# Performance work log

Hardware: AMD Instinct MI355X
Metric: run time of the kernel (lower is better)

The kernel has to match this reference:

```python
import jax, jax.numpy as jnp
import numpy as np

C = 64
CQ = C // 8
B, D, H, W = 4, 16, 16, 16


def setup_inputs() -> dict:
    key = jax.random.key(0)
    ks = jax.random.split(key, 8)
    s = 1.0 / np.sqrt(C)
    return {
        "x": jax.random.normal(ks[0], (B, C, D, H, W), jnp.float32),
        "Wq": jax.random.normal(ks[1], (CQ, C), jnp.float32) * s,
        "bq": jax.random.normal(ks[2], (CQ,), jnp.float32) * 0.01,
        "Wk": jax.random.normal(ks[3], (CQ, C), jnp.float32) * s,
        "bk": jax.random.normal(ks[4], (CQ,), jnp.float32) * 0.01,
        "Wv": jax.random.normal(ks[5], (C, C), jnp.float32) * s,
        "bv": jax.random.normal(ks[6], (C,), jnp.float32) * 0.01,
        "gamma": jnp.zeros((1,), jnp.float32) + 0.5,
    }


def reference(x, Wq, bq, Wk, bk, Wv, bv, gamma):
    b, c, d, h, w = x.shape
    n = d * h * w
    xf = x.reshape(b, c, n)  # [b, c, n]
    # 1x1x1 Conv3d == pointwise linear over channel dim
    q = jnp.einsum('oc,bcn->bon', Wq, xf) + bq[None, :, None]  # [b, cq, n]
    k = jnp.einsum('oc,bcn->bon', Wk, xf) + bk[None, :, None]  # [b, cq, n]
    v = jnp.einsum('oc,bcn->bon', Wv, xf) + bv[None, :, None]  # [b, c, n]
    # attn[b, i, j] = softmax_j(q[:, :, i] . k[:, :, j])
    scores = jnp.einsum('bci,bcj->bij', q, k)  # [b, n, n]
    attn = jax.nn.softmax(scores, axis=-1)
    # out = v @ attn^T : out[b, c, i] = sum_j v[b, c, j] * attn[b, i, j]
    out = jnp.einsum('bcj,bij->bci', v, attn).reshape(b, c, d, h, w)
    return gamma * out + x
```

## Files before the change

kernel.cpp:

```cpp
#include <hip/hip_runtime.h>
#include <hip/hip_bf16.h>
#include <cmath>

#define NTOK 4096

typedef float        f32x16 __attribute__((ext_vector_type(16)));
typedef short        s16x8  __attribute__((ext_vector_type(8)));
typedef unsigned int u32x4  __attribute__((ext_vector_type(4)));

__device__ __forceinline__ unsigned short f2bf(float f) {
    __hip_bfloat16 h = __float2bfloat16(f);
    return *reinterpret_cast<unsigned short*>(&h);
}
__device__ __forceinline__ float bf2f(unsigned short u) {
    __hip_bfloat16 h = *reinterpret_cast<__hip_bfloat16*>(&u);
    return __bfloat162float(h);
}
__device__ __forceinline__ unsigned pk2(float a, float b) {
    __hip_bfloat162 h = __float22bfloat162_rn(make_float2(a, b));
    return *reinterpret_cast<unsigned*>(&h);
}

__global__ __launch_bounds__(256)
void qkv_kernel(const float* __restrict__ x,
                const float* __restrict__ Wq, const float* __restrict__ bq,
                const float* __restrict__ Wk, const float* __restrict__ bk,
                const float* __restrict__ Wv, const float* __restrict__ bv,
                unsigned short* __restrict__ qt2, unsigned short* __restrict__ kt2,
                unsigned short* __restrict__ vt)
{
    __shared__ float wlds[16 * 64];
    __shared__ float blds[16];
    __shared__ float pacc[4][64][9];

    const int t    = threadIdx.x;
    const int lane = t & 63;
    const int wv   = t >> 6;
    const int part = blockIdx.x >> 8;
    const int vg   = blockIdx.x & 255;

    {
        const int row  = t >> 4;
        const int col4 = t & 15;
        const int g    = part * 16 + row;
        const float* src = (g < 8)  ? (Wq + g * 64)
                         : (g < 16) ? (Wk + (g - 8) * 64)
                                    : (Wv + (g - 16) * 64);
        ((float4*)wlds)[t] = ((const float4*)src)[col4];
        if (t < 16) {
            const int gg = part * 16 + t;
            blds[t] = (gg < 8) ? bq[gg] : (gg < 16) ? bk[gg - 8] : bv[gg - 16];
        }
    }
    __syncthreads();

    const int gid = vg * 64 + lane;
    const int b = gid >> 12;
    const int i = gid & (NTOK - 1);

    const float* xb = x + ((size_t)b * 64 + 16 * wv) * NTOK + i;
    float xv[16];
    #pragma unroll
    for (int c = 0; c < 16; c++) xv[c] = xb[(size_t)c * NTOK];

    const size_t row = (size_t)b * NTOK + i;
    const int jl   = i & 15;
    const int slot = (jl & 3) | ((jl & 4) << 1) | ((jl & 8) >> 1);

    #pragma unroll
    for (int ch = 0; ch < 2; ch++) {
        const int chunk = part * 2 + ch;

        float a[8];
        #pragma unroll
        for (int o = 0; o < 8; o++) a[o] = 0.f;
        #pragma unroll
        for (int c4 = 0; c4 < 4; c4++) {
            #pragma unroll
            for (int o = 0; o < 8; o++) {
                const float4 wv4 = ((const float4*)wlds)[(ch * 8 + o) * 16 + wv * 4 + c4];
                a[o] += wv4.x * xv[c4*4+0] + wv4.y * xv[c4*4+1]
                      + wv4.z * xv[c4*4+2] + wv4.w * xv[c4*4+3];
            }
        }
        if (ch) __syncthreads();
        #pragma unroll
        for (int o = 0; o < 8; o++) pacc[wv][lane][o] = a[o];
        __syncthreads();

        const int ob = 2 * wv;
        float fin[2];
        #pragma unroll
        for (int oo = 0; oo < 2; oo++)
            fin[oo] = ((pacc[0][lane][ob + oo] + pacc[1][lane][ob + oo])
                    +  (pacc[2][lane][ob + oo] + pacc[3][lane][ob + oo]))
                    + blds[ch * 8 + ob + oo];

        if (chunk < 2) {
            if (chunk == 0) {
                const float LOG2E = 1.4426950408889634f;
                fin[0] *= LOG2E; fin[1] *= LOG2E;
            }
            unsigned short hu[2], lu[2];
            #pragma unroll
            for (int oo = 0; oo < 2; oo++) {
                hu[oo] = f2bf(fin[oo]);
                lu[oo] = f2bf(fin[oo] - bf2f(hu[oo]));
            }
            unsigned short* dst = (chunk == 0 ? qt2 : kt2) + row * 16 + ob;
            *(unsigned*)dst       = *(const unsigned*)hu;
            *(unsigned*)(dst + 8) = *(const unsigned*)lu;
        } else {
            const int cbase = (chunk - 2) * 8 + ob;
            unsigned short* vdst =
                vt + ((size_t)b * 256 + (i >> 4)) * 1024 + (size_t)cbase * 16 + slot;
            vdst[0]  = f2bf(fin[0]);
            vdst[16] = f2bf(fin[1]);
        }
    }
}

__global__ __launch_bounds__(1024)
void attn_kernel(const unsigned short* __restrict__ qt2,
                 const unsigned short* __restrict__ kt2,
                 const unsigned short* __restrict__ vt,
                 const float* __restrict__ x,
                 const float* __restrict__ gamma,
                 float* __restrict__ out)
{
    __shared__ float slds[4][64][64];
    __shared__ float sldl[4][64];

    const int t    = threadIdx.x;
    const int l    = t & 63;
    const int wv   = t >> 6;
    const int qt   = wv & 1;
    const int u    = wv >> 1;
    const int lo31 = l & 31;
    const int h    = l >> 5;
    const int w     = blockIdx.x;
    const int b     = w >> 6;
    const int qbase = (w & 63) << 6;
    const int j0    = u << 9;

    const unsigned short* qrow =
        qt2 + ((size_t)b * NTOK + qbase + qt * 32 + lo31) * 16;
    s16x8 qB1 = *(const s16x8*)qrow;
    s16x8 qB2;
    if (h == 0) qB2 = *(const s16x8*)(qrow + 8);
    else        { u32x4 z = {0,0,0,0}; qB2 = __builtin_bit_cast(s16x8, z); }

    const unsigned short* kb  = kt2 + (size_t)b * NTOK * 16 + (size_t)h * 8;
    const unsigned short* vbA = vt + (size_t)b * NTOK * 64 + (size_t)lo31 * 16 + 8 * h;
    const unsigned short* vbB = vbA + 512;

    f32x16 accA, accB;
    #pragma unroll
    for (int r = 0; r < 16; r++) { accA[r] = 0.f; accB[r] = 0.f; }
    float lsum = 0.f;

    s16x8 K[2], V00[2], V01[2], V10[2], V11[2];

    #define LOADSET(s_, a_) do {                                              \
        K[s_]   = *(const s16x8*)(kb + (size_t)(j0 + ((a_) << 5) + lo31) * 16);  \
        V00[s_] = *(const s16x8*)(vbA + (size_t)((j0 >> 4) + ((a_) << 1)) * 1024);     \
        V01[s_] = *(const s16x8*)(vbA + (size_t)((j0 >> 4) + ((a_) << 1) + 1) * 1024); \
        V10[s_] = *(const s16x8*)(vbB + (size_t)((j0 >> 4) + ((a_) << 1)) * 1024);     \
        V11[s_] = *(const s16x8*)(vbB + (size_t)((j0 >> 4) + ((a_) << 1) + 1) * 1024); \
    } while (0)

    LOADSET(0, 0);

    #pragma unroll
    for (int it = 0; it < 16; ++it) {
        const int cu = it & 1;
        const int nx = it + 1;
        LOADSET(cu ^ 1, (nx < 16) ? nx : 0);

        f32x16 s;
        #pragma unroll
        for (int r = 0; r < 16; r++) s[r] = 0.f;
        s = __builtin_amdgcn_mfma_f32_32x32x16_bf16(K[cu], qB1, s, 0, 0, 0);
        s = __builtin_amdgcn_mfma_f32_32x32x16_bf16(K[cu], qB2, s, 0, 0, 0);

        #pragma unroll
        for (int r = 0; r < 16; r++) s[r] = __builtin_amdgcn_exp2f(s[r]);

        lsum += ((s[0]+s[1])+(s[2]+s[3])) + ((s[4]+s[5])+(s[6]+s[7]))
              + ((s[8]+s[9])+(s[10]+s[11])) + ((s[12]+s[13])+(s[14]+s[15]));

        u32x4 wa, wc;
        wa.x = pk2(s[0], s[1]);   wa.y = pk2(s[2], s[3]);
        wa.z = pk2(s[4], s[5]);   wa.w = pk2(s[6], s[7]);
        wc.x = pk2(s[8], s[9]);   wc.y = pk2(s[10], s[11]);
        wc.z = pk2(s[12], s[13]); wc.w = pk2(s[14], s[15]);
        s16x8 pf0 = __builtin_bit_cast(s16x8, wa);
        s16x8 pf1 = __builtin_bit_cast(s16x8, wc);

        __builtin_amdgcn_s_setprio(1);
        accA = __builtin_amdgcn_mfma_f32_32x32x16_bf16(V00[cu], pf0, accA, 0, 0, 0);
        accA = __builtin_amdgcn_mfma_f32_32x32x16_bf16(V01[cu], pf1, accA, 0, 0, 0);
        accB = __builtin_amdgcn_mfma_f32_32x32x16_bf16(V10[cu], pf0, accB, 0, 0, 0);
        accB = __builtin_amdgcn_mfma_f32_32x32x16_bf16(V11[cu], pf1, accB, 0, 0, 0);
        __builtin_amdgcn_s_setprio(0);
    }

    lsum += __shfl_xor(lsum, 32);

    #define WR_SLOT(sidx) do {                                                \
        const int s_ = (sidx);                                                \
        _Pragma("unroll")                                                     \
        for (int r = 0; r < 16; r++) {                                        \
            const int c_ = (r & 3) + 8 * (r >> 2) + 4 * h;                    \
            slds[s_][c_][qt * 32 + lo31]      = accA[r];                      \
            slds[s_][c_ + 32][qt * 32 + lo31] = accB[r];                      \
        }                                                                     \
        if (h == 0) sldl[s_][qt * 32 + lo31] = lsum;                          \
    } while (0)

    #define MRG_SLOT(sidx) do {                                               \
        const int s_ = (sidx);                                                \
        _Pragma("unroll")                                                     \
        for (int r = 0; r < 16; r++) {                                        \
            const int c_ = (r & 3) + 8 * (r >> 2) + 4 * h;                    \
            accA[r] += slds[s_][c_][qt * 32 + lo31];                          \
            accB[r] += slds[s_][c_ + 32][qt * 32 + lo31];                     \
        }                                                                     \
        lsum += sldl[s_][qt * 32 + lo31];                                     \
    } while (0)

    if (u >= 4) WR_SLOT(u - 4);
    __syncthreads();
    if (u < 4) MRG_SLOT(u);
    __syncthreads();
    if (u == 2 || u == 3) WR_SLOT(u - 2);
    __syncthreads();
    if (u < 2) MRG_SLOT(u);
    __syncthreads();
    if (u == 1) WR_SLOT(0);
    __syncthreads();
    if (u == 0) { MRG_SLOT(0); WR_SLOT(0); }
    __syncthreads();

    const int c  = t >> 4;
    const int q4 = (t & 15) << 2;
    const float g = gamma[0];
    const float4 a4 = *(const float4*)&slds[0][c][q4];
    const float g0 = g / sldl[0][q4 + 0];
    const float g1 = g / sldl[0][q4 + 1];
    const float g2 = g / sldl[0][q4 + 2];
    const float g3 = g / sldl[0][q4 + 3];
    const size_t off = (((size_t)b * 64 + c) << 12) + qbase + q4;
    const float4 xv4 = *(const float4*)(x + off);
    float4 o;
    o.x = a4.x * g0 + xv4.x;
    o.y = a4.y * g1 + xv4.y;
    o.z = a4.z * g2 + xv4.z;
    o.w = a4.w * g3 + xv4.w;
    *(float4*)(out + off) = o;
}

extern "C" void kernel_launch(void* const* d_in, const int* in_sizes, int n_in,
                              void* d_out, int out_size, void* d_ws, size_t ws_size,
                              hipStream_t stream) {
    const float* x     = (const float*)d_in[0];
    const float* Wq    = (const float*)d_in[1];
    const float* bq    = (const float*)d_in[2];
    const float* Wk    = (const float*)d_in[3];
    const float* bk    = (const float*)d_in[4];
    const float* Wv    = (const float*)d_in[5];
    const float* bv    = (const float*)d_in[6];
    const float* gamma = (const float*)d_in[7];
    float* out = (float*)d_out;

    unsigned short* qt2 = (unsigned short*)d_ws;
    unsigned short* kt2 = qt2 + (size_t)4 * NTOK * 16;
    unsigned short* vt  = kt2 + (size_t)4 * NTOK * 16;

    qkv_kernel<<<1280, 256, 0, stream>>>(x, Wq, bq, Wk, bk, Wv, bv, qt2, kt2, vt);
    attn_kernel<<<256, 1024, 0, stream>>>(qt2, kt2, vt, x, gamma, out);
}
```

Measured before the change: 31.93 us.

## Fuse QKV projection and attention into one kernel with grid barrier

Merges the projection kernel and the attention kernel into a single persistent launch of 256 blocks of 1024 threads. Each block computes all Q/K/V chunks for its 64 tokens, then a global atomic-counter barrier waits for every block before the attention phase, and shared memory is reused through a union. This removes one kernel launch and the gap between kernels, but adds a memset, a spin barrier that needs all 256 blocks resident at once, and a projection phase with fewer blocks than before.

```diff
diff --git a/kernel.cpp b/kernel.cpp
--- a/kernel.cpp
+++ b/kernel.cpp
@@ -3,6 +3,7 @@
 #include <cmath>
 
 #define NTOK 4096
+#define NBLK 256
 
 typedef float        f32x16 __attribute__((ext_vector_type(16)));
 typedef short        s16x8  __attribute__((ext_vector_type(8)));
@@ -21,137 +22,146 @@
     return *reinterpret_cast<unsigned*>(&h);
 }
 
-__global__ __launch_bounds__(256)
-void qkv_kernel(const float* __restrict__ x,
-                const float* __restrict__ Wq, const float* __restrict__ bq,
-                const float* __restrict__ Wk, const float* __restrict__ bk,
-                const float* __restrict__ Wv, const float* __restrict__ bv,
-                unsigned short* __restrict__ qt2, unsigned short* __restrict__ kt2,
-                unsigned short* __restrict__ vt)
+__global__ __launch_bounds__(1024)
+void fused_kernel(const float* __restrict__ x,
+                  const float* __restrict__ Wq, const float* __restrict__ bq,
+                  const float* __restrict__ Wk, const float* __restrict__ bk,
+                  const float* __restrict__ Wv, const float* __restrict__ bv,
+                  const float* __restrict__ gamma,
+                  unsigned short* qt2, unsigned short* kt2, unsigned short* vt,
+                  unsigned* bar, float* __restrict__ out)
 {
-    __shared__ float wlds[16 * 64];
-    __shared__ float blds[16];
-    __shared__ float pacc[4][64][9];
-
-    const int t    = threadIdx.x;
+    __shared__ union {
+        struct {
+            float w[80 * 64];
+            float bias[80];
+            float pacc[4][4][64][9];
+        } p1;
+        struct {
+            float slds[4][64][64];
+            float sldl[4][64];
+        } p2;
+    } sm;
+
+    const int t   = threadIdx.x;
+    const int blk = blockIdx.x;
     const int lane = t & 63;
     const int wv   = t >> 6;
-    const int part = blockIdx.x >> 8;
-    const int vg   = blockIdx.x & 255;
 
     {
-        const int row  = t >> 4;
-        const int col4 = t & 15;
-        const int g    = part * 16 + row;
-        const float* src = (g < 8)  ? (Wq + g * 64)
-                         : (g < 16) ? (Wk + (g - 8) * 64)
-                                    : (Wv + (g - 16) * 64);
-        ((float4*)wlds)[t] = ((const float4*)src)[col4];
-        if (t < 16) {
-            const int gg = part * 16 + t;
-            blds[t] = (gg < 8) ? bq[gg] : (gg < 16) ? bk[gg - 8] : bv[gg - 16];
+        for (int idx = t; idx < 1280; idx += 1024) {
+            const int row  = idx >> 4;
+            const int col4 = idx & 15;
+            const float* src = (row < 8)  ? (Wq + row * 64)
+                             : (row < 16) ? (Wk + (row - 8) * 64)
+                                          : (Wv + (row - 16) * 64);
+            ((float4*)sm.p1.w)[idx] = ((const float4*)src)[col4];
+        }
+        if (t < 80)
+            sm.p1.bias[t] = (t < 8) ? bq[t] : (t < 16) ? bk[t - 8] : bv[t - 16];
+        __syncthreads();
+
+        const int cq = wv & 3;
+        const int cp = wv >> 2;
+        const int gid = blk * 64 + lane;
+        const int b = gid >> 12;
+        const int i = gid & (NTOK - 1);
+
+        const float* xb = x + ((size_t)b * 64 + 16 * cq) * NTOK + i;
+        float xv[16];
+        #pragma unroll
+        for (int c = 0; c < 16; c++) xv[c] = xb[(size_t)c * NTOK];
+
+        const size_t row = (size_t)b * NTOK + i;
+        const int jl   = i & 15;
+        const int slot = (jl & 3) | ((jl & 4) << 1) | ((jl & 8) >> 1);
+
+        #pragma unroll
+        for (int s = 0; s < 3; ++s) {
+            const int chunk = cp + 4 * s;
+            const bool act = (chunk < 10);
+            if (act) {
+                float a[8];
+                #pragma unroll
+                for (int o = 0; o < 8; o++) a[o] = 0.f;
+                #pragma unroll
+                for (int c4 = 0; c4 < 4; c4++) {
+                    #pragma unroll
+                    for (int o = 0; o < 8; o++) {
+                        const float4 w4v =
+                            ((const float4*)sm.p1.w)[(chunk * 8 + o) * 16 + cq * 4 + c4];
+                        a[o] += w4v.x * xv[c4*4+0] + w4v.y * xv[c4*4+1]
+                              + w4v.z * xv[c4*4+2] + w4v.w * xv[c4*4+3];
+                    }
+                }
+                #pragma unroll
+                for (int o = 0; o < 8; o++) sm.p1.pacc[cp][cq][lane][o] = a[o];
+            }
+            __syncthreads();
+            if (act) {
+                const int ob = 2 * cq;
+                float fin[2];
+                #pragma unroll
+                for (int oo = 0; oo < 2; oo++)
+                    fin[oo] = ((sm.p1.pacc[cp][0][lane][ob + oo]
+                              + sm.p1.pacc[cp][1][lane][ob + oo])
+                             + (sm.p1.pacc[cp][2][lane][ob + oo]
+                              + sm.p1.pacc[cp][3][lane][ob + oo]))
+                            + sm.p1.bias[chunk * 8 + ob + oo];
+
+                if (chunk < 2) {
+                    if (chunk == 0) {
+                        const float LOG2E = 1.4426950408889634f;
+                        fin[0] *= LOG2E; fin[1] *= LOG2E;
+                    }
+                    unsigned short hu[2], lu[2];
+                    #pragma unroll
+                    for (int oo = 0; oo < 2; oo++) {
+                        hu[oo] = f2bf(fin[oo]);
+                        lu[oo] = f2bf(fin[oo] - bf2f(hu[oo]));
+                    }
+                    unsigned short* dst = (chunk == 0 ? qt2 : kt2) + row * 16 + ob;
+                    *(unsigned*)dst       = *(const unsigned*)hu;
+                    *(unsigned*)(dst + 8) = *(const unsigned*)lu;
+                } else {
+                    const int cbase = (chunk - 2) * 8 + ob;
+                    unsigned short* vdst =
+                        vt + ((size_t)b * 256 + (i >> 4)) * 1024 + (size_t)cbase * 16 + slot;
+                    vdst[0]  = f2bf(fin[0]);
+                    vdst[16] = f2bf(fin[1]);
+                }
+            }
+            if (s < 2) __syncthreads();
         }
     }
-    __syncthreads();
-
-    const int gid = vg * 64 + lane;
-    const int b = gid >> 12;
-    const int i = gid & (NTOK - 1);
-
-    const float* xb = x + ((size_t)b * 64 + 16 * wv) * NTOK + i;
-    float xv[16];
-    #pragma unroll
-    for (int c = 0; c < 16; c++) xv[c] = xb[(size_t)c * NTOK];
-
-    const size_t row = (size_t)b * NTOK + i;
-    const int jl   = i & 15;
-    const int slot = (jl & 3) | ((jl & 4) << 1) | ((jl & 8) >> 1);
-
-    #pragma unroll
-    for (int ch = 0; ch < 2; ch++) {
-        const int chunk = part * 2 + ch;
-
-        float a[8];
-        #pragma unroll
-        for (int o = 0; o < 8; o++) a[o] = 0.f;
-        #pragma unroll
-        for (int c4 = 0; c4 < 4; c4++) {
-            #pragma unroll
-            for (int o = 0; o < 8; o++) {
-                const float4 wv4 = ((const float4*)wlds)[(ch * 8 + o) * 16 + wv * 4 + c4];
-                a[o] += wv4.x * xv[c4*4+0] + wv4.y * xv[c4*4+1]
-                      + wv4.z * xv[c4*4+2] + wv4.w * xv[c4*4+3];
-            }
-        }
-        if (ch) __syncthreads();
-        #pragma unroll
-        for (int o = 0; o < 8; o++) pacc[wv][lane][o] = a[o];
-        __syncthreads();
-
-        const int ob = 2 * wv;
-        float fin[2];
-        #pragma unroll
-        for (int oo = 0; oo < 2; oo++)
-            fin[oo] = ((pacc[0][lane][ob + oo] + pacc[1][lane][ob + oo])
-                    +  (pacc[2][lane][ob + oo] + pacc[3][lane][ob + oo]))
-                    + blds[ch * 8 + ob + oo];
-
-        if (chunk < 2) {
-            if (chunk == 0) {
-                const float LOG2E = 1.4426950408889634f;
-                fin[0] *= LOG2E; fin[1] *= LOG2E;
-            }
-            unsigned short hu[2], lu[2];
-            #pragma unroll
-            for (int oo = 0; oo < 2; oo++) {
-                hu[oo] = f2bf(fin[oo]);
-                lu[oo] = f2bf(fin[oo] - bf2f(hu[oo]));
-            }
-            unsigned short* dst = (chunk == 0 ? qt2 : kt2) + row * 16 + ob;
-            *(unsigned*)dst       = *(const unsigned*)hu;
-            *(unsigned*)(dst + 8) = *(const unsigned*)lu;
-        } else {
-            const int cbase = (chunk - 2) * 8 + ob;
-            unsigned short* vdst =
-                vt + ((size_t)b * 256 + (i >> 4)) * 1024 + (size_t)cbase * 16 + slot;
-            vdst[0]  = f2bf(fin[0]);
-            vdst[16] = f2bf(fin[1]);
-        }
+
+    __syncthreads();
+    if (t == 0) {
+        __threadfence();
+        atomicAdd(bar, 1u);
+        while (atomicOr(bar, 0u) < NBLK)
+            __builtin_amdgcn_s_sleep(16);
+        __threadfence();
     }
-}
-
-__global__ __launch_bounds__(1024)
-void attn_kernel(const unsigned short* __restrict__ qt2,
-                 const unsigned short* __restrict__ kt2,
-                 const unsigned short* __restrict__ vt,
-                 const float* __restrict__ x,
-                 const float* __restrict__ gamma,
-                 float* __restrict__ out)
-{
-    __shared__ float slds[4][64][64];
-    __shared__ float sldl[4][64];
-
-    const int t    = threadIdx.x;
-    const int l    = t & 63;
-    const int wv   = t >> 6;
+    __syncthreads();
+
     const int qt   = wv & 1;
     const int u    = wv >> 1;
-    const int lo31 = l & 31;
-    const int h    = l >> 5;
-    const int w     = blockIdx.x;
-    const int b     = w >> 6;
-    const int qbase = (w & 63) << 6;
+    const int lo31 = lane & 31;
+    const int h    = lane >> 5;
+    const int b2    = blk >> 6;
+    const int qbase = (blk & 63) << 6;
     const int j0    = u << 9;
 
     const unsigned short* qrow =
-        qt2 + ((size_t)b * NTOK + qbase + qt * 32 + lo31) * 16;
+        qt2 + ((size_t)b2 * NTOK + qbase + qt * 32 + lo31) * 16;
     s16x8 qB1 = *(const s16x8*)qrow;
     s16x8 qB2;
     if (h == 0) qB2 = *(const s16x8*)(qrow + 8);
     else        { u32x4 z = {0,0,0,0}; qB2 = __builtin_bit_cast(s16x8, z); }
 
-    const unsigned short* kb  = kt2 + (size_t)b * NTOK * 16 + (size_t)h * 8;
-    const unsigned short* vbA = vt + (size_t)b * NTOK * 64 + (size_t)lo31 * 16 + 8 * h;
+    const unsigned short* kb  = kt2 + (size_t)b2 * NTOK * 16 + (size_t)h * 8;
+    const unsigned short* vbA = vt + (size_t)b2 * NTOK * 64 + (size_t)lo31 * 16 + 8 * h;
     const unsigned short* vbB = vbA + 512;
 
     f32x16 accA, accB;
@@ -212,10 +222,10 @@
         _Pragma("unroll")                                                     \
         for (int r = 0; r < 16; r++) {                                        \
             const int c_ = (r & 3) + 8 * (r >> 2) + 4 * h;                    \
-            slds[s_][c_][qt * 32 + lo31]      = accA[r];                      \
-            slds[s_][c_ + 32][qt * 32 + lo31] = accB[r];                      \
+            sm.p2.slds[s_][c_][qt * 32 + lo31]      = accA[r];                \
+            sm.p2.slds[s_][c_ + 32][qt * 32 + lo31] = accB[r];                \
         }                                                                     \
-        if (h == 0) sldl[s_][qt * 32 + lo31] = lsum;                          \
+        if (h == 0) sm.p2.sldl[s_][qt * 32 + lo31] = lsum;                    \
     } while (0)
 
     #define MRG_SLOT(sidx) do {                                               \
@@ -223,10 +233,10 @@
         _Pragma("unroll")                                                     \
         for (int r = 0; r < 16; r++) {                                        \
             const int c_ = (r & 3) + 8 * (r >> 2) + 4 * h;                    \
-            accA[r] += slds[s_][c_][qt * 32 + lo31];                          \
-            accB[r] += slds[s_][c_ + 32][qt * 32 + lo31];                     \
+            accA[r] += sm.p2.slds[s_][c_][qt * 32 + lo31];                    \
+            accB[r] += sm.p2.slds[s_][c_ + 32][qt * 32 + lo31];               \
         }                                                                     \
-        lsum += sldl[s_][qt * 32 + lo31];                                     \
+        lsum += sm.p2.sldl[s_][qt * 32 + lo31];                               \
     } while (0)
 
     if (u >= 4) WR_SLOT(u - 4);
@@ -245,12 +255,12 @@
     const int c  = t >> 4;
     const int q4 = (t & 15) << 2;
     const float g = gamma[0];
-    const float4 a4 = *(const float4*)&slds[0][c][q4];
-    const float g0 = g / sldl[0][q4 + 0];
-    const float g1 = g / sldl[0][q4 + 1];
-    const float g2 = g / sldl[0][q4 + 2];
-    const float g3 = g / sldl[0][q4 + 3];
-    const size_t off = (((size_t)b * 64 + c) << 12) + qbase + q4;
+    const float4 a4 = *(const float4*)&sm.p2.slds[0][c][q4];
+    const float g0 = g / sm.p2.sldl[0][q4 + 0];
+    const float g1 = g / sm.p2.sldl[0][q4 + 1];
+    const float g2 = g / sm.p2.sldl[0][q4 + 2];
+    const float g3 = g / sm.p2.sldl[0][q4 + 3];
+    const size_t off = (((size_t)b2 * 64 + c) << 12) + qbase + q4;
     const float4 xv4 = *(const float4*)(x + off);
     float4 o;
     o.x = a4.x * g0 + xv4.x;
@@ -276,7 +286,9 @@
     unsigned short* qt2 = (unsigned short*)d_ws;
     unsigned short* kt2 = qt2 + (size_t)4 * NTOK * 16;
     unsigned short* vt  = kt2 + (size_t)4 * NTOK * 16;
-
-    qkv_kernel<<<1280, 256, 0, stream>>>(x, Wq, bq, Wk, bk, Wv, bv, qt2, kt2, vt);
-    attn_kernel<<<256, 1024, 0, stream>>>(qt2, kt2, vt, x, gamma, out);
-}
+    unsigned* bar = (unsigned*)(vt + (size_t)4 * 64 * NTOK);
+
+    hipMemsetAsync(bar, 0, 8, stream);
+    fused_kernel<<<NBLK, 1024, 0, stream>>>(x, Wq, bq, Wk, bk, Wv, bv, gamma,
+                                            qt2, kt2, vt, bar, out);
+}
```

Measured after the change: 59.83 us. 1.87x slower.
